# Performance work log

Measured on AMD Instinct MI355X. Metric: run time of the kernel, lower is better.

The kernel has to match this reference:

```python
import jax, jax.numpy as jnp
import numpy as np

N, E, DIN, DOUT = 50000, 800000, 256, 256
P = DOUT // 2  # attention projection dim = feature_dim // 2


def _mlp2(x, W1, b1, W2, b2):
    # nn.Sequential(Linear, ReLU, Linear)
    return jax.nn.relu(x @ W1 + b1) @ W2 + b2


def _spmm(indices, values, x):
    # y[r] = sum_e values[e] * x[col[e]] for edges with row[e] == r
    rows, cols = indices[0], indices[1]
    return jax.ops.segment_sum(values[:, None] * x[cols], rows, num_segments=x.shape[0])


def setup_inputs() -> dict:
    key = jax.random.key(0)
    ks = iter(jax.random.split(key, 64))

    def nrm(shape, scale=0.05):
        return jax.random.normal(next(ks), shape, jnp.float32) * scale

    inp = {}
    inp["features"] = jax.random.normal(next(ks), (N, DIN), jnp.float32)
    inp["edge_features"] = jax.random.normal(next(ks), (N, DOUT), jnp.float32)
    for i in (1, 2, 3, 4):
        inp[f"adj{i}_indices"] = jax.random.randint(next(ks), (2, E), 0, N)
        inp[f"adj{i}_values"] = jax.random.uniform(next(ks), (E,), jnp.float32)
    # feature_transform: Linear(in, out)
    inp["ft_W"] = nrm((DIN, DOUT)); inp["ft_b"] = jnp.zeros((DOUT,), jnp.float32)
    # six 2-layer MLPs: first_order(fo), edge(em), second(so), third(to), fourth(qo), final(m)
    for p in ("fo", "em", "so", "to", "qo", "m"):
        inp[f"{p}_W1"] = nrm((DOUT, DOUT)); inp[f"{p}_b1"] = jnp.zeros((DOUT,), jnp.float32)
        inp[f"{p}_W2"] = nrm((DOUT, DOUT)); inp[f"{p}_b2"] = jnp.zeros((DOUT,), jnp.float32)
    # attention query/key projections to DOUT//2
    inp["q_W"] = nrm((DOUT, P)); inp["q_b"] = jnp.zeros((P,), jnp.float32)
    inp["k_W"] = nrm((DOUT, P)); inp["k_b"] = jnp.zeros((P,), jnp.float32)
    return inp


def reference(features, edge_features,
              adj1_indices, adj1_values, adj2_indices, adj2_values,
              adj3_indices, adj3_values, adj4_indices, adj4_values,
              ft_W, ft_b,
              fo_W1, fo_b1, fo_W2, fo_b2,
              em_W1, em_b1, em_W2, em_b2,
              so_W1, so_b1, so_W2, so_b2,
              to_W1, to_b1, to_W2, to_b2,
              qo_W1, qo_b1, qo_W2, qo_b2,
              m_W1, m_b1, m_W2, m_b2,
              q_W, q_b, k_W, k_b):
    feats = features @ ft_W + ft_b                                    # [N, DOUT]
    # first order: spmm -> MLP, then add spmm of edge-MLP features
    fo = _mlp2(_spmm(adj1_indices, adj1_values, feats), fo_W1, fo_b1, fo_W2, fo_b2)
    ef = _mlp2(edge_features, em_W1, em_b1, em_W2, em_b2)
    fo = fo + _spmm(adj1_indices, adj1_values, ef)
    # higher orders: spmm -> MLP + residual
    so_agg = _spmm(adj2_indices, adj2_values, feats)
    so = _mlp2(so_agg, so_W1, so_b1, so_W2, so_b2) + so_agg
    to_agg = _spmm(adj3_indices, adj3_values, feats)
    to = _mlp2(to_agg, to_W1, to_b1, to_W2, to_b2) + to_agg
    qo_agg = _spmm(adj4_indices, adj4_values, feats)
    qo = _mlp2(qo_agg, qo_W1, qo_b1, qo_W2, qo_b2) + qo_agg
    # attention combination over the 5 feature sets
    all_f = jnp.stack([feats, fo, so, to, qo], axis=1)                # [N, 5, DOUT]
    q = feats @ q_W + q_b                                             # [N, P]
    keys = all_f @ k_W + k_b                                          # [N, 5, P]
    scores = jnp.einsum('np,nkp->nk', q, keys)                        # [N, 5]
    w = jax.nn.softmax(scores, axis=-1)
    combined = jnp.einsum('nk,nkd->nd', w, all_f)                     # [N, DOUT]
    # final MLP (dropout is identity in eval mode)
    return _mlp2(combined, m_W1, m_b1, m_W2, m_b2)
```

## Files before the change

kernel.cpp:

```cpp
#include <hip/hip_runtime.h>


#define DO 256

typedef unsigned short u16;
typedef _Float16 f16;
typedef __attribute__((ext_vector_type(8))) _Float16 f16x8;
typedef __attribute__((ext_vector_type(4))) _Float16 f16x4;
typedef __attribute__((ext_vector_type(4))) float f32x4;


struct WDesc { const float* src; f16* dst; };
struct WPack { WDesc w[13]; };
struct CsrSrc { const int* rows[4]; const int* cols[4]; const float* vals[4]; int E[4]; };

__global__ __launch_bounds__(256) void prep_kernel(
    CsrSrc cs, int* __restrict__ cnt, int NPo, WPack wp,
    const float* __restrict__ qW, const float* __restrict__ kW,
    const float* __restrict__ qb, f16* __restrict__ pdst, float* __restrict__ pb)
{
    int y = blockIdx.y;
    if (y < 4) {
        int e = blockIdx.x * 256 + threadIdx.x;
        if (e < cs.E[y]) atomicAdd(&cnt[(size_t)y * NPo + cs.rows[y][e]], 1);
        return;
    }
    if (y < 17) {
        if (blockIdx.x >= 256) return;
        WDesc d = wp.w[y - 4];
        int idx = blockIdx.x * 256 + threadIdx.x;
        int e  = idx & 7;
        int l  = (idx >> 3) & 63;
        int ks = (idx >> 9) & 7;
        int f  = idx >> 12;
        int c  = (f << 4) | (l & 15);
        int k  = ks * 32 + ((l >> 4) << 3) + e;
        d.dst[idx] = (f16)d.src[k * 256 + c];
        return;
    }
    if (y == 17) {
        if (blockIdx.x >= 256) return;
        int idx = blockIdx.x * 256 + threadIdx.x;
        int e  = idx & 7;
        int l  = (idx >> 3) & 63;
        int ks = (idx >> 9) & 7;
        int f  = idx >> 12;
        int c  = (f << 4) | (l & 15);
        int k  = ks * 32 + ((l >> 4) << 3) + e;
        float s = 0.f;
        #pragma unroll 8
        for (int p = 0; p < 128; ++p) s += qW[k * 128 + p] * kW[c * 128 + p];
        pdst[idx] = (f16)s;
        return;
    }
    if (blockIdx.x != 0) return;
    int c = threadIdx.x;
    float s = 0.f;
    #pragma unroll 8
    for (int p = 0; p < 128; ++p) s += qb[p] * kW[c * 128 + p];
    pb[c] = s;
}

__global__ __launch_bounds__(1024) void scan4_kernel(
    const int* __restrict__ cnt0, int* __restrict__ off0, int N, int NPo)
{
    const int* cnt = cnt0 + (size_t)blockIdx.x * NPo;
    int* off = off0 + (size_t)blockIdx.x * NPo;
    __shared__ int part[1024];
    const int t = threadIdx.x;
    const int chunk = (N + 1023) / 1024;
    const int lo = t * chunk;
    const int hi = min(lo + chunk, N);
    int s = 0;
    for (int i = lo; i < hi; ++i) s += cnt[i];
    part[t] = s;
    __syncthreads();
    for (int d = 1; d < 1024; d <<= 1) {
        int u = (t >= d) ? part[t - d] : 0;
        __syncthreads();
        part[t] += u;
        __syncthreads();
    }
    int running = part[t] - s;
    for (int i = lo; i < hi; ++i) { off[i] = running; running += cnt[i]; }
    if (t == 1023) off[N] = part[1023];
}

static __device__ __forceinline__ void stage_A(
    char* smem, const f16* A, const float* A32, int brow, int N, int tid)
{
    #pragma unroll
    for (int j = 0; j < 8; ++j) {
        int i = tid + j * 256;
        int row = i >> 5, slot = i & 31;
        int srow = brow + row; srow = srow < N ? srow : N - 1;
        f16x8 v;
        if (A32) {
            const float* s = &A32[(size_t)srow * 256 + slot * 8];
            float4 v0 = *(const float4*)s;
            float4 v1 = *(const float4*)(s + 4);
            v = f16x8{(f16)v0.x, (f16)v0.y, (f16)v0.z, (f16)v0.w,
                      (f16)v1.x, (f16)v1.y, (f16)v1.z, (f16)v1.w};
        } else {
            v = *(const f16x8*)&A[(size_t)srow * 256 + slot * 8];
        }
        int db = (row * 512 + slot * 16) ^ ((row & 7) << 4);
        *(f16x8*)(smem + db) = v;
    }
}

static __device__ __forceinline__ void gemm_from_lds(
    const char* smem, const f16* W, f32x4 (&acc)[4][4],
    int wave, int lane, int lrow, int kg)
{
    #pragma unroll
    for (int ks = 0; ks < 8; ++ks) {
        f16x8 ah[4], bh[4];
        #pragma unroll
        for (int m = 0; m < 4; ++m) {
            int ab = ((m * 16 + lrow) * 512 + (ks * 4 + kg) * 16) ^ ((lrow & 7) << 4);
            ah[m] = *(const f16x8*)(smem + ab);
        }
        #pragma unroll
        for (int n = 0; n < 4; ++n)
            bh[n] = *(const f16x8*)&W[(size_t)(((wave * 4 + n) * 8 + ks) << 9) + (lane << 3)];
        #pragma unroll
        for (int m = 0; m < 4; ++m)
            #pragma unroll
            for (int n = 0; n < 4; ++n)
                acc[m][n] = __builtin_amdgcn_mfma_f32_16x16x32_f16(
                                ah[m], bh[n], acc[m][n], 0, 0, 0);
    }
}

static __device__ __forceinline__ void mlp_from_lds(
    char* smem, const f16* W1, const float* b1, const f16* W2,
    f32x4 (&acc)[4][4], int wave, int lane, int lrow, int kg)
{
    const int wc = wave * 64;
    gemm_from_lds(smem, W1, acc, wave, lane, lrow, kg);
    __syncthreads();
    #pragma unroll
    for (int n = 0; n < 4; ++n) {
        int c = wc + n * 16 + lrow;
        float bv = b1[c];
        #pragma unroll
        for (int m = 0; m < 4; ++m)
            #pragma unroll
            for (int j = 0; j < 4; ++j) {
                int rl = m * 16 + kg * 4 + j;
                float v = fmaxf(acc[m][n][j] + bv, 0.f);
                int hb = (rl * 512 + c * 2) ^ ((rl & 7) << 4);
                *(f16*)(smem + hb) = (f16)v;
            }
    }
    __syncthreads();
    #pragma unroll
    for (int m = 0; m < 4; ++m)
        #pragma unroll
        for (int n = 0; n < 4; ++n)
            acc[m][n] = f32x4{0.f, 0.f, 0.f, 0.f};
    gemm_from_lds(smem, W2, acc, wave, lane, lrow, kg);
}

static __device__ __forceinline__ void fused_mlp_body(
    char* smem, const f16* A, const float* A32,
    const f16* W1, const float* b1, const f16* W2, const float* b2,
    const f16* Ad, f16* Ch, float* Cf, int N, int brow)
{
    const int tid  = threadIdx.x;
    const int wave = tid >> 6, lane = tid & 63;
    const int lrow = lane & 15, kg = lane >> 4;
    const int wc   = wave * 64;

    stage_A(smem, A, A32, brow, N, tid);
    __syncthreads();

    f32x4 acc[4][4] = {};
    mlp_from_lds(smem, W1, b1, W2, acc, wave, lane, lrow, kg);

    #pragma unroll
    for (int n = 0; n < 4; ++n) {
        int c = wc + n * 16 + lrow;
        float bv = b2[c];
        #pragma unroll
        for (int m = 0; m < 4; ++m)
            #pragma unroll
            for (int j = 0; j < 4; ++j) {
                int r = brow + m * 16 + kg * 4 + j;
                if (r >= N) continue;
                size_t o = (size_t)r * 256 + c;
                float v = acc[m][n][j] + bv;
                if (Ad) v += (float)Ad[o];
                if (Cf) Cf[o] = v;
                else    Ch[o] = (f16)v;
            }
    }
}

static __device__ __forceinline__ void gemm1_body(
    char* smem, const float* A32, const f16* W1, const float* b1,
    f16* Ch, int N, int brow)
{
    const int tid  = threadIdx.x;
    const int wave = tid >> 6, lane = tid & 63;
    const int lrow = lane & 15, kg = lane >> 4;
    const int wc   = wave * 64;

    stage_A(smem, nullptr, A32, brow, N, tid);
    __syncthreads();
    f32x4 acc[4][4] = {};
    gemm_from_lds(smem, W1, acc, wave, lane, lrow, kg);

    #pragma unroll
    for (int n = 0; n < 4; ++n) {
        int c = wc + n * 16 + lrow;
        float bv = b1[c];
        #pragma unroll
        for (int m = 0; m < 4; ++m)
            #pragma unroll
            for (int j = 0; j < 4; ++j) {
                int r = brow + m * 16 + kg * 4 + j;
                if (r >= N) continue;
                Ch[(size_t)r * 256 + c] = (f16)(acc[m][n][j] + bv);
            }
    }
}

__global__ __launch_bounds__(256) void stage2_kernel(
    CsrSrc cs, const int* __restrict__ off, int* __restrict__ cur,
    int2* __restrict__ se, int NPo, int Emax,
    const float* __restrict__ features, const float* __restrict__ edge_features,
    const f16* __restrict__ w_ft, const float* __restrict__ ft_b,
    const f16* __restrict__ w_em1, const float* __restrict__ em_b1,
    const f16* __restrict__ w_em2, const float* __restrict__ em_b2,
    f16* __restrict__ F, f16* __restrict__ ef, int N)
{
    __shared__ char smem[32768];
    int y = blockIdx.y;
    if (y < 4) {
        int e = blockIdx.x * 256 + threadIdx.x;
        if (e >= cs.E[y]) return;
        int r = cs.rows[y][e];
        int p = off[(size_t)y * NPo + r] + atomicAdd(&cur[(size_t)y * NPo + r], 1);
        se[(size_t)y * Emax + p] = make_int2(cs.cols[y][e],
                                             __float_as_int(cs.vals[y][e]));
        return;
    }
    int gx = blockIdx.x;
    if (gx >= (N + 63) / 64) return;
    if (y == 4)
        gemm1_body(smem, features, w_ft, ft_b, F, N, gx * 64);
    else
        fused_mlp_body(smem, nullptr, edge_features, w_em1, em_b1, w_em2, em_b2,
                       nullptr, ef, nullptr, N, gx * 64);
}

struct Spmm5 {
    const int* off; const int2* se; int NPo; int Emax;
    const f16* F; const f16* ef;
    f16* out[5];
};
__global__ __launch_bounds__(256) void spmm5_kernel(Spmm5 s, int N) {
    int y = blockIdx.y;
    int r = blockIdx.x * 4 + (threadIdx.x >> 6);
    if (r >= N) return;
    int lane = threadIdx.x & 63;
    int a = (y <= 1) ? 0 : y - 1;
    const int* off = s.off + (size_t)a * s.NPo;
    const int2* se = s.se + (size_t)a * s.Emax;
    const f16* X = (y == 1) ? s.ef : s.F;
    f16* Y = s.out[y];
    int e0 = off[r], e1 = off[r + 1];

    float a0 = 0.f, a1 = 0.f, a2 = 0.f, a3 = 0.f;
    int e = e0;
    for (; e + 3 < e1; e += 4) {
        int2 ev0 = se[e], ev1 = se[e + 1], ev2 = se[e + 2], ev3 = se[e + 3];
        f16x4 x0 = *(const f16x4*)&X[(size_t)ev0.x * DO + lane * 4];
        f16x4 x1 = *(const f16x4*)&X[(size_t)ev1.x * DO + lane * 4];
        f16x4 x2 = *(const f16x4*)&X[(size_t)ev2.x * DO + lane * 4];
        f16x4 x3 = *(const f16x4*)&X[(size_t)ev3.x * DO + lane * 4];
        float v0 = __int_as_float(ev0.y), v1 = __int_as_float(ev1.y);
        float v2 = __int_as_float(ev2.y), v3 = __int_as_float(ev3.y);
        a0 = fmaf(v0, (float)x0[0], a0); a1 = fmaf(v0, (float)x0[1], a1);
        a2 = fmaf(v0, (float)x0[2], a2); a3 = fmaf(v0, (float)x0[3], a3);
        a0 = fmaf(v1, (float)x1[0], a0); a1 = fmaf(v1, (float)x1[1], a1);
        a2 = fmaf(v1, (float)x1[2], a2); a3 = fmaf(v1, (float)x1[3], a3);
        a0 = fmaf(v2, (float)x2[0], a0); a1 = fmaf(v2, (float)x2[1], a1);
        a2 = fmaf(v2, (float)x2[2], a2); a3 = fmaf(v2, (float)x2[3], a3);
        a0 = fmaf(v3, (float)x3[0], a0); a1 = fmaf(v3, (float)x3[1], a1);
        a2 = fmaf(v3, (float)x3[2], a2); a3 = fmaf(v3, (float)x3[3], a3);
    }
    for (; e < e1; ++e) {
        int2 ev = se[e];
        float v = __int_as_float(ev.y);
        f16x4 x = *(const f16x4*)&X[(size_t)ev.x * DO + lane * 4];
        a0 = fmaf(v, (float)x[0], a0); a1 = fmaf(v, (float)x[1], a1);
        a2 = fmaf(v, (float)x[2], a2); a3 = fmaf(v, (float)x[3], a3);
    }
    f16x4 o = {(f16)a0, (f16)a1, (f16)a2, (f16)a3};
    *(f16x4*)&Y[(size_t)r * DO + lane * 4] = o;
}

struct Mlp4 {
    const f16* a[4]; const f16* ad[4];
    const f16* w1[4]; const f16* w2[4];
    const float* b1[4]; const float* b2[4];
    f16* out[4];
};
__global__ __launch_bounds__(256) void mlp4_kernel(Mlp4 p, int N) {
    __shared__ char smem[32768];
    int y = blockIdx.y;
    fused_mlp_body(smem, p.a[y], nullptr, p.w1[y], p.b1[y], p.w2[y], p.b2[y],
                   p.ad[y], p.out[y], nullptr, N, blockIdx.x * 64);
}

__global__ __launch_bounds__(256) void score_combine_mlp_kernel(
    const f16* __restrict__ F, const f16* __restrict__ P,
    const float* __restrict__ pb,
    const f16* __restrict__ F1, const f16* __restrict__ F2,
    const f16* __restrict__ F3, const f16* __restrict__ F4,
    const f16* __restrict__ mW1, const float* __restrict__ mb1,
    const f16* __restrict__ mW2, const float* __restrict__ mb2,
    float* __restrict__ Out, int N)
{
    __shared__ char smem[32768];
    __shared__ float sred[4][64][5];
    __shared__ float w5[64][5];

    const int tid  = threadIdx.x;
    const int wave = tid >> 6, lane = tid & 63;
    const int lrow = lane & 15, kg = lane >> 4;
    const int wc   = wave * 64;
    const int brow = blockIdx.x * 64;

    stage_A(smem, F, nullptr, brow, N, tid);
    __syncthreads();

    f32x4 acc[4][4] = {};
    gemm_from_lds(smem, P, acc, wave, lane, lrow, kg);

    #pragma unroll
    for (int m = 0; m < 4; ++m) {
        #pragma unroll
        for (int j = 0; j < 4; ++j) {
            int rl = m * 16 + kg * 4 + j;
            int r  = brow + rl;
            float p0 = 0.f, p1 = 0.f, p2 = 0.f, p3 = 0.f, p4 = 0.f;
            if (r < N) {
                #pragma unroll
                for (int n = 0; n < 4; ++n) {
                    int c = wc + n * 16 + lrow;
                    float v = acc[m][n][j] + pb[c];
                    int ab = (rl * 512 + c * 2) ^ ((rl & 7) << 4);
                    float f0 = (float)*(const f16*)(smem + ab);
                    size_t fo = (size_t)r * 256 + c;
                    p0 += v * f0;
                    p1 += v * (float)F1[fo];
                    p2 += v * (float)F2[fo];
                    p3 += v * (float)F3[fo];
                    p4 += v * (float)F4[fo];
                }
            }
            #pragma unroll
            for (int d = 1; d < 16; d <<= 1) {
                p0 += __shfl_xor(p0, d, 64);
                p1 += __shfl_xor(p1, d, 64);
                p2 += __shfl_xor(p2, d, 64);
                p3 += __shfl_xor(p3, d, 64);
                p4 += __shfl_xor(p4, d, 64);
            }
            if (lrow == 0) {
                sred[wave][rl][0] = p0; sred[wave][rl][1] = p1;
                sred[wave][rl][2] = p2; sred[wave][rl][3] = p3;
                sred[wave][rl][4] = p4;
            }
        }
    }
    __syncthreads();

    if (tid < 64) {
        float s[5];
        #pragma unroll
        for (int k = 0; k < 5; ++k)
            s[k] = sred[0][tid][k] + sred[1][tid][k] + sred[2][tid][k] + sred[3][tid][k];
        float mx = fmaxf(fmaxf(fmaxf(s[0], s[1]), fmaxf(s[2], s[3])), s[4]);
        float sum = 0.f;
        #pragma unroll
        for (int k = 0; k < 5; ++k) { s[k] = expf(s[k] - mx); sum += s[k]; }
        float inv = 1.f / sum;
        #pragma unroll
        for (int k = 0; k < 5; ++k) w5[tid][k] = s[k] * inv;
    }
    __syncthreads();

    #pragma unroll
    for (int m = 0; m < 4; ++m) {
        #pragma unroll
        for (int j = 0; j < 4; ++j) {
            int rl = m * 16 + kg * 4 + j;
            int r  = brow + rl;
            float w0 = w5[rl][0], w1 = w5[rl][1], w2 = w5[rl][2],
                  w3 = w5[rl][3], w4 = w5[rl][4];
            #pragma unroll
            for (int n = 0; n < 4; ++n) {
                int c = wc + n * 16 + lrow;
                int ab = (rl * 512 + c * 2) ^ ((rl & 7) << 4);
                float f0 = (float)*(const f16*)(smem + ab);
                float res = f0;
                if (r < N) {
                    size_t fo = (size_t)r * 256 + c;
                    res = w0 * f0
                        + w1 * (float)F1[fo]
                        + w2 * (float)F2[fo]
                        + w3 * (float)F3[fo]
                        + w4 * (float)F4[fo];
                }
                *(f16*)(smem + ab) = (f16)res;
            }
        }
    }
    __syncthreads();

    #pragma unroll
    for (int m = 0; m < 4; ++m)
        #pragma unroll
        for (int n = 0; n < 4; ++n)
            acc[m][n] = f32x4{0.f, 0.f, 0.f, 0.f};
    mlp_from_lds(smem, mW1, mb1, mW2, acc, wave, lane, lrow, kg);

    #pragma unroll
    for (int n = 0; n < 4; ++n) {
        int c = wc + n * 16 + lrow;
        float bv = mb2[c];
        #pragma unroll
        for (int m = 0; m < 4; ++m)
            #pragma unroll
            for (int j = 0; j < 4; ++j) {
                int r = brow + m * 16 + kg * 4 + j;
                if (r >= N) continue;
                Out[(size_t)r * 256 + c] = acc[m][n][j] + bv;
            }
    }
}

extern "C" void kernel_launch(void* const* d_in, const int* in_sizes, int n_in,
                              void* d_out, int out_size, void* d_ws, size_t ws_size,
                              hipStream_t stream)
{
    const float* features      = (const float*)d_in[0];
    const float* edge_features = (const float*)d_in[1];
    CsrSrc cs;
    for (int i = 0; i < 4; ++i) {
        const int* idx = (const int*)d_in[2 + 2 * i];
        cs.E[i]    = in_sizes[3 + 2 * i];
        cs.rows[i] = idx;
        cs.cols[i] = idx + cs.E[i];
        cs.vals[i] = (const float*)d_in[3 + 2 * i];
    }
    const int Emax = max(max(cs.E[0], cs.E[1]), max(cs.E[2], cs.E[3]));

    const float* ft_W = (const float*)d_in[10]; const float* ft_b = (const float*)d_in[11];
    const float* fo_W1 = (const float*)d_in[12]; const float* fo_b1 = (const float*)d_in[13];
    const float* fo_W2 = (const float*)d_in[14]; const float* fo_b2 = (const float*)d_in[15];
    const float* em_W1 = (const float*)d_in[16]; const float* em_b1 = (const float*)d_in[17];
    const float* em_W2 = (const float*)d_in[18]; const float* em_b2 = (const float*)d_in[19];
    const float* so_W1 = (const float*)d_in[20]; const float* so_b1 = (const float*)d_in[21];
    const float* so_W2 = (const float*)d_in[22]; const float* so_b2 = (const float*)d_in[23];
    const float* to_W1 = (const float*)d_in[24]; const float* to_b1 = (const float*)d_in[25];
    const float* to_W2 = (const float*)d_in[26]; const float* to_b2 = (const float*)d_in[27];
    const float* qo_W1 = (const float*)d_in[28]; const float* qo_b1 = (const float*)d_in[29];
    const float* qo_W2 = (const float*)d_in[30]; const float* qo_b2 = (const float*)d_in[31];
    const float* m_W1  = (const float*)d_in[32]; const float* m_b1  = (const float*)d_in[33];
    const float* m_W2  = (const float*)d_in[34]; const float* m_b2  = (const float*)d_in[35];
    const float* q_W   = (const float*)d_in[36]; const float* q_b   = (const float*)d_in[37];
    const float* k_W   = (const float*)d_in[38]; const float* k_b   = (const float*)d_in[39];
    (void)k_b;

    const int N = in_sizes[0] / 256;
    const size_t NS = (size_t)N * DO;

    char* base = (char*)d_ws;
    size_t o = 0;
    auto take = [&](size_t bytes) { char* p = base + o; o += (bytes + 63) & ~(size_t)63; return p; };
    const int NPo = (N + 64) & ~63;
    int*  cnt = (int*)take((size_t)4 * NPo * 4);
    int*  cur = (int*)take((size_t)4 * NPo * 4);
    int*  off = (int*)take((size_t)4 * NPo * 4);
    int2* se  = (int2*)take((size_t)4 * Emax * 8);
    f16* B1 = (f16*)take(NS * 2);
    f16* B2 = (f16*)take(NS * 2);
    f16* B3 = (f16*)take(NS * 2);
    f16* B4 = (f16*)take(NS * 2);
    f16* B5 = (f16*)take(NS * 2);
    f16* B6 = (f16*)take(NS * 2);
    f16* B7 = (f16*)take(NS * 2);
    const size_t WSQ = 65536;
    f16* WT = (f16*)take(14 * WSQ * 2);
    float* pb = (float*)take(256 * 4);
    if (o > ws_size) return;

    f16* F = B4;

    f16* w[14];
    for (int i = 0; i < 14; ++i) w[i] = WT + (size_t)i * WSQ;

    dim3 blk(256);
    const int EG = (Emax + 255) / 256;
    const int GG = (N + 63) / 64;

    hipMemsetAsync(cnt, 0, (size_t)8 * NPo * 4, stream);

    {
        WPack wp;
        const float* src[13] = {ft_W, fo_W1, fo_W2, em_W1, em_W2, so_W1, so_W2,
                                to_W1, to_W2, qo_W1, qo_W2, m_W1, m_W2};
        for (int i = 0; i < 13; ++i) { wp.w[i].src = src[i]; wp.w[i].dst = w[i]; }
        hipLaunchKernelGGL(prep_kernel, dim3(EG, 19), blk, 0, stream,
                           cs, cnt, NPo, wp, q_W, k_W, q_b, w[13], pb);
    }
    hipLaunchKernelGGL(scan4_kernel, dim3(4), dim3(1024), 0, stream, cnt, off, N, NPo);
    hipLaunchKernelGGL(stage2_kernel, dim3(EG, 6), blk, 0, stream,
                       cs, off, cur, se, NPo, Emax,
                       features, edge_features,
                       w[0], ft_b, w[3], em_b1, w[4], em_b2, F, B3, N);
    {
        Spmm5 sp;
        sp.off = off; sp.se = se; sp.NPo = NPo; sp.Emax = Emax;
        sp.F = F; sp.ef = B3;
        sp.out[0] = B1; sp.out[1] = B2; sp.out[2] = B5; sp.out[3] = B6; sp.out[4] = B7;
        hipLaunchKernelGGL(spmm5_kernel, dim3((N + 3) / 4, 5), blk, 0, stream, sp, N);
    }
    {
        Mlp4 p;
        const f16* a[4]  = {B1, B5, B6, B7};
        const f16* ad[4] = {B2, B5, B6, B7};
        f16* out[4]      = {B1, B5, B6, B7};
        int wi1[4] = {1, 5, 7, 9}, wi2[4] = {2, 6, 8, 10};
        const float* bb1[4] = {fo_b1, so_b1, to_b1, qo_b1};
        const float* bb2[4] = {fo_b2, so_b2, to_b2, qo_b2};
        for (int i = 0; i < 4; ++i) {
            p.a[i] = a[i]; p.ad[i] = ad[i]; p.out[i] = out[i];
            p.w1[i] = w[wi1[i]]; p.w2[i] = w[wi2[i]];
            p.b1[i] = bb1[i]; p.b2[i] = bb2[i];
        }
        hipLaunchKernelGGL(mlp4_kernel, dim3(GG, 4), blk, 0, stream, p, N);
    }
    hipLaunchKernelGGL(score_combine_mlp_kernel, dim3(GG), blk, 0, stream,
                       F, w[13], pb, B1, B5, B6, B7,
                       w[11], m_b1, w[12], m_b2, (float*)d_out, N);
}
```

Baseline: 1.075 ms.

## Fuse SpMM gather into per-order MLP kernel, coarsen edge-processing threads

Replaces the separate spmm5 and mlp4 kernels with one kernel that gathers each 64-row tile's aggregation straight into LDS and runs the two-layer MLP on it. The adj1 path gathers both feats and edge features in a single pass and keeps the residual for the final add. This is meant to remove the global write and re-read of four aggregated intermediates and one launch. It also makes each edge-processing thread in the prep and CSR-fill stages handle four edges instead of one. The cost is fewer waves doing the latency-bound gather per block, since each wave walks 16 rows one after another, which may lower memory-level parallelism.

```diff
diff --git a/kernel.cpp b/kernel.cpp
--- a/kernel.cpp
+++ b/kernel.cpp
@@ -21,8 +21,12 @@
 {
     int y = blockIdx.y;
     if (y < 4) {
-        int e = blockIdx.x * 256 + threadIdx.x;
-        if (e < cs.E[y]) atomicAdd(&cnt[(size_t)y * NPo + cs.rows[y][e]], 1);
+        int base = blockIdx.x * 1024 + threadIdx.x;
+        #pragma unroll
+        for (int k = 0; k < 4; ++k) {
+            int e = base + k * 256;
+            if (e < cs.E[y]) atomicAdd(&cnt[(size_t)y * NPo + cs.rows[y][e]], 1);
+        }
         return;
     }
     if (y < 17) {
@@ -239,12 +243,17 @@
     __shared__ char smem[32768];
     int y = blockIdx.y;
     if (y < 4) {
-        int e = blockIdx.x * 256 + threadIdx.x;
-        if (e >= cs.E[y]) return;
-        int r = cs.rows[y][e];
-        int p = off[(size_t)y * NPo + r] + atomicAdd(&cur[(size_t)y * NPo + r], 1);
-        se[(size_t)y * Emax + p] = make_int2(cs.cols[y][e],
-                                             __float_as_int(cs.vals[y][e]));
+        int base = blockIdx.x * 1024 + threadIdx.x;
+        #pragma unroll
+        for (int k = 0; k < 4; ++k) {
+            int e = base + k * 256;
+            if (e < cs.E[y]) {
+                int r = cs.rows[y][e];
+                int p = off[(size_t)y * NPo + r] + atomicAdd(&cur[(size_t)y * NPo + r], 1);
+                se[(size_t)y * Emax + p] = make_int2(cs.cols[y][e],
+                                                     __float_as_int(cs.vals[y][e]));
+            }
+        }
         return;
     }
     int gx = blockIdx.x;
@@ -256,64 +265,165 @@
                        nullptr, ef, nullptr, N, gx * 64);
 }
 
-struct Spmm5 {
+struct SpmmMlp4 {
     const int* off; const int2* se; int NPo; int Emax;
     const f16* F; const f16* ef;
-    f16* out[5];
-};
-__global__ __launch_bounds__(256) void spmm5_kernel(Spmm5 s, int N) {
-    int y = blockIdx.y;
-    int r = blockIdx.x * 4 + (threadIdx.x >> 6);
-    if (r >= N) return;
-    int lane = threadIdx.x & 63;
-    int a = (y <= 1) ? 0 : y - 1;
-    const int* off = s.off + (size_t)a * s.NPo;
-    const int2* se = s.se + (size_t)a * s.Emax;
-    const f16* X = (y == 1) ? s.ef : s.F;
-    f16* Y = s.out[y];
-    int e0 = off[r], e1 = off[r + 1];
-
-    float a0 = 0.f, a1 = 0.f, a2 = 0.f, a3 = 0.f;
-    int e = e0;
-    for (; e + 3 < e1; e += 4) {
-        int2 ev0 = se[e], ev1 = se[e + 1], ev2 = se[e + 2], ev3 = se[e + 3];
-        f16x4 x0 = *(const f16x4*)&X[(size_t)ev0.x * DO + lane * 4];
-        f16x4 x1 = *(const f16x4*)&X[(size_t)ev1.x * DO + lane * 4];
-        f16x4 x2 = *(const f16x4*)&X[(size_t)ev2.x * DO + lane * 4];
-        f16x4 x3 = *(const f16x4*)&X[(size_t)ev3.x * DO + lane * 4];
-        float v0 = __int_as_float(ev0.y), v1 = __int_as_float(ev1.y);
-        float v2 = __int_as_float(ev2.y), v3 = __int_as_float(ev3.y);
-        a0 = fmaf(v0, (float)x0[0], a0); a1 = fmaf(v0, (float)x0[1], a1);
-        a2 = fmaf(v0, (float)x0[2], a2); a3 = fmaf(v0, (float)x0[3], a3);
-        a0 = fmaf(v1, (float)x1[0], a0); a1 = fmaf(v1, (float)x1[1], a1);
-        a2 = fmaf(v1, (float)x1[2], a2); a3 = fmaf(v1, (float)x1[3], a3);
-        a0 = fmaf(v2, (float)x2[0], a0); a1 = fmaf(v2, (float)x2[1], a1);
-        a2 = fmaf(v2, (float)x2[2], a2); a3 = fmaf(v2, (float)x2[3], a3);
-        a0 = fmaf(v3, (float)x3[0], a0); a1 = fmaf(v3, (float)x3[1], a1);
-        a2 = fmaf(v3, (float)x3[2], a2); a3 = fmaf(v3, (float)x3[3], a3);
-    }
-    for (; e < e1; ++e) {
-        int2 ev = se[e];
-        float v = __int_as_float(ev.y);
-        f16x4 x = *(const f16x4*)&X[(size_t)ev.x * DO + lane * 4];
-        a0 = fmaf(v, (float)x[0], a0); a1 = fmaf(v, (float)x[1], a1);
-        a2 = fmaf(v, (float)x[2], a2); a3 = fmaf(v, (float)x[3], a3);
-    }
-    f16x4 o = {(f16)a0, (f16)a1, (f16)a2, (f16)a3};
-    *(f16x4*)&Y[(size_t)r * DO + lane * 4] = o;
-}
-
-struct Mlp4 {
-    const f16* a[4]; const f16* ad[4];
+    f16* aggef;
     const f16* w1[4]; const f16* w2[4];
     const float* b1[4]; const float* b2[4];
     f16* out[4];
 };
-__global__ __launch_bounds__(256) void mlp4_kernel(Mlp4 p, int N) {
+__global__ __launch_bounds__(256) void spmm_mlp4_kernel(SpmmMlp4 p, int N) {
     __shared__ char smem[32768];
-    int y = blockIdx.y;
-    fused_mlp_body(smem, p.a[y], nullptr, p.w1[y], p.b1[y], p.w2[y], p.b2[y],
-                   p.ad[y], p.out[y], nullptr, N, blockIdx.x * 64);
+    const int y = blockIdx.y;
+    const int brow = blockIdx.x * 64;
+    const int tid  = threadIdx.x;
+    const int wave = tid >> 6, lane = tid & 63;
+    const int lrow = lane & 15, kg = lane >> 4;
+    const int wc   = wave * 64;
+
+    const int* off = p.off + (size_t)y * p.NPo;
+    const int2* se = p.se + (size_t)y * p.Emax;
+
+    for (int rr = 0; rr < 16; ++rr) {
+        int rl = wave * 16 + rr;
+        int r  = brow + rl;
+        float a0 = 0.f, a1 = 0.f, a2 = 0.f, a3 = 0.f;
+        float c0 = 0.f, c1 = 0.f, c2 = 0.f, c3 = 0.f;
+        if (r < N) {
+            int e0 = off[r], e1 = off[r + 1];
+            if (y == 0) {
+                int e = e0;
+                for (; e + 1 < e1; e += 2) {
+                    int2 ev0 = se[e], ev1 = se[e + 1];
+                    float v0 = __int_as_float(ev0.y), v1 = __int_as_float(ev1.y);
+                    size_t x0o = (size_t)ev0.x * DO + lane * 4;
+                    size_t x1o = (size_t)ev1.x * DO + lane * 4;
+                    f16x4 f0 = *(const f16x4*)&p.F[x0o];
+                    f16x4 g0 = *(const f16x4*)&p.ef[x0o];
+                    f16x4 f1 = *(const f16x4*)&p.F[x1o];
+                    f16x4 g1 = *(const f16x4*)&p.ef[x1o];
+                    a0 = fmaf(v0, (float)f0[0], a0); a1 = fmaf(v0, (float)f0[1], a1);
+                    a2 = fmaf(v0, (float)f0[2], a2); a3 = fmaf(v0, (float)f0[3], a3);
+                    c0 = fmaf(v0, (float)g0[0], c0); c1 = fmaf(v0, (float)g0[1], c1);
+                    c2 = fmaf(v0, (float)g0[2], c2); c3 = fmaf(v0, (float)g0[3], c3);
+                    a0 = fmaf(v1, (float)f1[0], a0); a1 = fmaf(v1, (float)f1[1], a1);
+                    a2 = fmaf(v1, (float)f1[2], a2); a3 = fmaf(v1, (float)f1[3], a3);
+                    c0 = fmaf(v1, (float)g1[0], c0); c1 = fmaf(v1, (float)g1[1], c1);
+                    c2 = fmaf(v1, (float)g1[2], c2); c3 = fmaf(v1, (float)g1[3], c3);
+                }
+                if (e < e1) {
+                    int2 ev = se[e];
+                    float v = __int_as_float(ev.y);
+                    size_t xo = (size_t)ev.x * DO + lane * 4;
+                    f16x4 f0 = *(const f16x4*)&p.F[xo];
+                    f16x4 g0 = *(const f16x4*)&p.ef[xo];
+                    a0 = fmaf(v, (float)f0[0], a0); a1 = fmaf(v, (float)f0[1], a1);
+                    a2 = fmaf(v, (float)f0[2], a2); a3 = fmaf(v, (float)f0[3], a3);
+                    c0 = fmaf(v, (float)g0[0], c0); c1 = fmaf(v, (float)g0[1], c1);
+                    c2 = fmaf(v, (float)g0[2], c2); c3 = fmaf(v, (float)g0[3], c3);
+                }
+            } else {
+                int e = e0;
+                for (; e + 3 < e1; e += 4) {
+                    int2 ev0 = se[e], ev1 = se[e + 1], ev2 = se[e + 2], ev3 = se[e + 3];
+                    f16x4 x0 = *(const f16x4*)&p.F[(size_t)ev0.x * DO + lane * 4];
+                    f16x4 x1 = *(const f16x4*)&p.F[(size_t)ev1.x * DO + lane * 4];
+                    f16x4 x2 = *(const f16x4*)&p.F[(size_t)ev2.x * DO + lane * 4];
+                    f16x4 x3 = *(const f16x4*)&p.F[(size_t)ev3.x * DO + lane * 4];
+                    float v0 = __int_as_float(ev0.y), v1 = __int_as_float(ev1.y);
+                    float v2 = __int_as_float(ev2.y), v3 = __int_as_float(ev3.y);
+                    a0 = fmaf(v0, (float)x0[0], a0); a1 = fmaf(v0, (float)x0[1], a1);
+                    a2 = fmaf(v0, (float)x0[2], a2); a3 = fmaf(v0, (float)x0[3], a3);
+                    a0 = fmaf(v1, (float)x1[0], a0); a1 = fmaf(v1, (float)x1[1], a1);
+                    a2 = fmaf(v1, (float)x1[2], a2); a3 = fmaf(v1, (float)x1[3], a3);
+                    a0 = fmaf(v2, (float)x2[0], a0); a1 = fmaf(v2, (float)x2[1], a1);
+                    a2 = fmaf(v2, (float)x2[2], a2); a3 = fmaf(v2, (float)x2[3], a3);
+                    a0 = fmaf(v3, (float)x3[0], a0); a1 = fmaf(v3, (float)x3[1], a1);
+                    a2 = fmaf(v3, (float)x3[2], a2); a3 = fmaf(v3, (float)x3[3], a3);
+                }
+                for (; e < e1; ++e) {
+                    int2 ev = se[e];
+                    float v = __int_as_float(ev.y);
+                    f16x4 x = *(const f16x4*)&p.F[(size_t)ev.x * DO + lane * 4];
+                    a0 = fmaf(v, (float)x[0], a0); a1 = fmaf(v, (float)x[1], a1);
+                    a2 = fmaf(v, (float)x[2], a2); a3 = fmaf(v, (float)x[3], a3);
+                }
+            }
+        }
+        int addr = ((rl * 512 + (lane >> 1) * 16) ^ ((rl & 7) << 4)) + (lane & 1) * 8;
+        f16x4 o = {(f16)a0, (f16)a1, (f16)a2, (f16)a3};
+        *(f16x4*)(smem + addr) = o;
+        if (y == 0 && r < N) {
+            f16x4 og = {(f16)c0, (f16)c1, (f16)c2, (f16)c3};
+            *(f16x4*)&p.aggef[(size_t)r * 256 + lane * 4] = og;
+        }
+    }
+    __syncthreads();
+
+    f32x4 acc[4][4] = {};
+    gemm_from_lds(smem, p.w1[y], acc, wave, lane, lrow, kg);
+
+    f16x4 res[4][4];
+    if (y >= 1) {
+        #pragma unroll
+        for (int m = 0; m < 4; ++m)
+            #pragma unroll
+            for (int n = 0; n < 4; ++n) {
+                int c = wc + n * 16 + lrow;
+                #pragma unroll
+                for (int j = 0; j < 4; ++j) {
+                    int rl2 = m * 16 + kg * 4 + j;
+                    int ab = (rl2 * 512 + c * 2) ^ ((rl2 & 7) << 4);
+                    res[m][n][j] = *(const f16*)(smem + ab);
+                }
+            }
+    }
+    __syncthreads();
+
+    const float* b1 = p.b1[y];
+    #pragma unroll
+    for (int n = 0; n < 4; ++n) {
+        int c = wc + n * 16 + lrow;
+        float bv = b1[c];
+        #pragma unroll
+        for (int m = 0; m < 4; ++m)
+            #pragma unroll
+            for (int j = 0; j < 4; ++j) {
+                int rl2 = m * 16 + kg * 4 + j;
+                float v = fmaxf(acc[m][n][j] + bv, 0.f);
+                int hb = (rl2 * 512 + c * 2) ^ ((rl2 & 7) << 4);
+                *(f16*)(smem + hb) = (f16)v;
+            }
+    }
+    __syncthreads();
+
+    #pragma unroll
+    for (int m = 0; m < 4; ++m)
+        #pragma unroll
+        for (int n = 0; n < 4; ++n)
+            acc[m][n] = f32x4{0.f, 0.f, 0.f, 0.f};
+    gemm_from_lds(smem, p.w2[y], acc, wave, lane, lrow, kg);
+
+    const float* b2 = p.b2[y];
+    f16* out = p.out[y];
+    #pragma unroll
+    for (int n = 0; n < 4; ++n) {
+        int c = wc + n * 16 + lrow;
+        float bv = b2[c];
+        #pragma unroll
+        for (int m = 0; m < 4; ++m)
+            #pragma unroll
+            for (int j = 0; j < 4; ++j) {
+                int r = brow + m * 16 + kg * 4 + j;
+                if (r >= N) continue;
+                size_t o = (size_t)r * 256 + c;
+                float v = acc[m][n][j] + bv;
+                if (y == 0) v += (float)p.aggef[o];
+                else        v += (float)res[m][n][j];
+                out[o] = (f16)v;
+            }
+    }
 }
 
 __global__ __launch_bounds__(256) void score_combine_mlp_kernel(
@@ -507,8 +617,10 @@
     for (int i = 0; i < 14; ++i) w[i] = WT + (size_t)i * WSQ;
 
     dim3 blk(256);
-    const int EG = (Emax + 255) / 256;
-    const int GG = (N + 63) / 64;
+    const int EG4 = (Emax + 1023) / 1024;
+    const int GG  = (N + 63) / 64;
+    const int PX  = (EG4 > 256) ? EG4 : 256;
+    const int SX  = (EG4 > GG) ? EG4 : GG;
 
     hipMemsetAsync(cnt, 0, (size_t)8 * NPo * 4, stream);
 
@@ -517,35 +629,27 @@
         const float* src[13] = {ft_W, fo_W1, fo_W2, em_W1, em_W2, so_W1, so_W2,
                                 to_W1, to_W2, qo_W1, qo_W2, m_W1, m_W2};
         for (int i = 0; i < 13; ++i) { wp.w[i].src = src[i]; wp.w[i].dst = w[i]; }
-        hipLaunchKernelGGL(prep_kernel, dim3(EG, 19), blk, 0, stream,
+        hipLaunchKernelGGL(prep_kernel, dim3(PX, 19), blk, 0, stream,
                            cs, cnt, NPo, wp, q_W, k_W, q_b, w[13], pb);
     }
     hipLaunchKernelGGL(scan4_kernel, dim3(4), dim3(1024), 0, stream, cnt, off, N, NPo);
-    hipLaunchKernelGGL(stage2_kernel, dim3(EG, 6), blk, 0, stream,
+    hipLaunchKernelGGL(stage2_kernel, dim3(SX, 6), blk, 0, stream,
                        cs, off, cur, se, NPo, Emax,
                        features, edge_features,
                        w[0], ft_b, w[3], em_b1, w[4], em_b2, F, B3, N);
     {
-        Spmm5 sp;
-        sp.off = off; sp.se = se; sp.NPo = NPo; sp.Emax = Emax;
-        sp.F = F; sp.ef = B3;
-        sp.out[0] = B1; sp.out[1] = B2; sp.out[2] = B5; sp.out[3] = B6; sp.out[4] = B7;
-        hipLaunchKernelGGL(spmm5_kernel, dim3((N + 3) / 4, 5), blk, 0, stream, sp, N);
-    }
-    {
-        Mlp4 p;
-        const f16* a[4]  = {B1, B5, B6, B7};
-        const f16* ad[4] = {B2, B5, B6, B7};
-        f16* out[4]      = {B1, B5, B6, B7};
+        SpmmMlp4 p;
+        p.off = off; p.se = se; p.NPo = NPo; p.Emax = Emax;
+        p.F = F; p.ef = B3; p.aggef = B2;
         int wi1[4] = {1, 5, 7, 9}, wi2[4] = {2, 6, 8, 10};
         const float* bb1[4] = {fo_b1, so_b1, to_b1, qo_b1};
         const float* bb2[4] = {fo_b2, so_b2, to_b2, qo_b2};
+        f16* out[4] = {B1, B5, B6, B7};
         for (int i = 0; i < 4; ++i) {
-            p.a[i] = a[i]; p.ad[i] = ad[i]; p.out[i] = out[i];
             p.w1[i] = w[wi1[i]]; p.w2[i] = w[wi2[i]];
-            p.b1[i] = bb1[i]; p.b2[i] = bb2[i];
-        }
-        hipLaunchKernelGGL(mlp4_kernel, dim3(GG, 4), blk, 0, stream, p, N);
+            p.b1[i] = bb1[i]; p.b2[i] = bb2[i]; p.out[i] = out[i];
+        }
+        hipLaunchKernelGGL(spmm_mlp4_kernel, dim3(GG, 4), blk, 0, stream, p, N);
     }
     hipLaunchKernelGGL(score_combine_mlp_kernel, dim3(GG), blk, 0, stream,
                        F, w[13], pb, B1, B5, B6, B7,
```

Result: slower. 1.687 ms (+57.0%).
